# Performance work log

Hardware: AMD Instinct MI355X
Metric: run time of the kernel (lower is better)

Reference implementation:

```python
import jax, jax.numpy as jnp
import numpy as np

N_NODES = 10000
N_EDGES = 160000
BATCH = 32
IN_FEAT = 64
POLY_K = 5
OUT_FEAT = 128


def setup_inputs() -> dict:
    key = jax.random.key(0)
    k_x, k_r, k_c, k_v, k_w, k_b = jax.random.split(key, 6)
    x = jax.random.normal(k_x, (BATCH, N_NODES, IN_FEAT), dtype=jnp.float32)
    lap_rows = jax.random.randint(k_r, (N_EDGES,), 0, N_NODES, dtype=jnp.int32)
    lap_cols = jax.random.randint(k_c, (N_EDGES,), 0, N_NODES, dtype=jnp.int32)
    # small values keep the degree-5 Chebyshev recurrence numerically tame
    lap_vals = jax.random.normal(k_v, (N_EDGES,), dtype=jnp.float32) * 0.05
    weight = jax.random.normal(k_w, (IN_FEAT * POLY_K, OUT_FEAT), dtype=jnp.float32) * 0.1
    bias = jax.random.normal(k_b, (1, 1, OUT_FEAT), dtype=jnp.float32) * 0.1
    return {"x": x, "lap_rows": lap_rows, "lap_cols": lap_cols,
            "lap_vals": lap_vals, "weight": weight, "bias": bias,
            "pooling_size": 4}


def _spmm(rows, cols, vals, m):
    # sparse [N,N] @ dense [N,M] via gather + segment_sum
    return jax.ops.segment_sum(vals[:, None] * m[cols], rows, num_segments=N_NODES)


def reference(x, lap_rows, lap_cols, lap_vals, weight, bias, pooling_size):
    B, N, F = x.shape
    K = POLY_K
    Fo = weight.shape[1]
    # x0: [N, F*B]
    x0 = jnp.transpose(x, (1, 2, 0)).reshape(N, F * B)
    terms = [x0]
    if K > 1:
        x1 = _spmm(lap_rows, lap_cols, lap_vals, x0)
        terms.append(x1)
        for _ in range(2, K):
            x2 = 2.0 * _spmm(lap_rows, lap_cols, lap_vals, x1) - x0
            terms.append(x2)
            x0, x1 = x1, x2
    xk = jnp.stack(terms, axis=0)                      # [K, N, F*B]
    xk = xk.reshape(K, N, F, B)
    xk = jnp.transpose(xk, (3, 1, 2, 0))               # [B, N, F, K]
    xk = xk.reshape(B * N, F * K)
    out = (xk @ weight).reshape(B, N, Fo)              # dense projection
    out = jax.nn.relu(out + bias)                      # bias + ReLU
    if pooling_size > 1:
        out = out.reshape(B, N // pooling_size, pooling_size, Fo).max(axis=2)
    return out
```

## Files before the change

kernel.cpp:

```cpp
#include <hip/hip_runtime.h>
#include <hip/hip_bf16.h>
#include <cstddef>
#include <cstdint>

#define N_NODES 10000
#define N_EDGES 160000
#define BATCH 32
#define IN_FEAT 64
#define POLY_K 5
#define OUT_FEAT 128
#define KTOT 320
#define POOLSZ 4
#define NPOOL 2500
#define NSL 16

typedef short bf16x8 __attribute__((ext_vector_type(8)));
typedef unsigned short u16x8 __attribute__((ext_vector_type(8)));
typedef unsigned int u32x4 __attribute__((ext_vector_type(4)));
typedef float f32x4 __attribute__((ext_vector_type(4)));
typedef float f32x2 __attribute__((ext_vector_type(2)));

__device__ __forceinline__ unsigned short f2bf(float f) {
  unsigned int u = __float_as_uint(f);
  unsigned int r = u + 0x7FFFu + ((u >> 16) & 1u);
  return (unsigned short)(r >> 16);
}
__device__ __forceinline__ float bf2f(unsigned short u) {
  return __uint_as_float(((unsigned int)u) << 16);
}
__device__ __forceinline__ f32x2 unpk(unsigned int u) {
  f32x2 r;
  r[0] = __uint_as_float(u << 16);
  r[1] = __uint_as_float(u & 0xFFFF0000u);
  return r;
}


__global__ void zero_int_kernel(int* __restrict__ p, int n) {
  int i = blockIdx.x * 256 + threadIdx.x;
  if (i < n) p[i] = 0;
}

__global__ void hist_kernel(const int* __restrict__ rows, int* __restrict__ deg) {
  int e = blockIdx.x * 256 + threadIdx.x;
  if (e < N_EDGES) atomicAdd(&deg[rows[e]], 1);
}

__global__ void scan_kernel(const int* __restrict__ deg, int* __restrict__ row_start,
                            int* __restrict__ cursor) {
  __shared__ int wsum[16];
  __shared__ int carry_sm;
  int t = threadIdx.x;
  int lane = t & 63, wid = t >> 6;
  if (t == 0) { carry_sm = 0; row_start[0] = 0; }
  __syncthreads();
  for (int base = 0; base < N_NODES; base += 1024) {
    int idx = base + t;
    int v = (idx < N_NODES) ? deg[idx] : 0;
    int x = v;
    #pragma unroll
    for (int off = 1; off < 64; off <<= 1) {
      int y = __shfl_up(x, off, 64);
      if (lane >= off) x += y;
    }
    if (lane == 63) wsum[wid] = x;
    __syncthreads();
    if (wid == 0) {
      int sv = (lane < 16) ? wsum[lane] : 0;
      #pragma unroll
      for (int off = 1; off < 16; off <<= 1) {
        int y = __shfl_up(sv, off, 64);
        if (lane >= off) sv += y;
      }
      if (lane < 16) wsum[lane] = sv;
    }
    __syncthreads();
    int incl = x + (wid > 0 ? wsum[wid - 1] : 0) + carry_sm;
    if (idx < N_NODES) {
      row_start[idx + 1] = incl;
      cursor[idx] = incl - v;
    }
    __syncthreads();
    if (t == 1023) carry_sm = incl;
    __syncthreads();
  }
}

__global__ void scatter_kernel(const int* __restrict__ rows, const int* __restrict__ cols,
                               const float* __restrict__ vals, int* __restrict__ cursor,
                               int2* __restrict__ csr_pairs) {
  int e = blockIdx.x * 256 + threadIdx.x;
  if (e < N_EDGES) {
    int r = rows[e];
    int p = atomicAdd(&cursor[r], 1);
    csr_pairs[p] = make_int2(cols[e], __float_as_int(vals[e]));
  }
}


__global__ void bsort_kernel(const int* __restrict__ deg, int* __restrict__ perm) {
  int chunk = blockIdx.x * 256 + threadIdx.x;
  if (chunk >= (N_NODES + 15) / 16) return;
  int base = chunk * 16;
  int idx[16], dg[16];
  #pragma unroll
  for (int j = 0; j < 16; ++j) {
    int r = base + j;
    idx[j] = r;
    dg[j] = (r < N_NODES) ? deg[r] : 0x7fffffff;
  }
  #pragma unroll
  for (int a = 1; a < 16; ++a) {
    int dv = dg[a], iv = idx[a];
    int b = a - 1;
    while (b >= 0 && dg[b] > dv) { dg[b + 1] = dg[b]; idx[b + 1] = idx[b]; --b; }
    dg[b + 1] = dv; idx[b + 1] = iv;
  }
  #pragma unroll
  for (int j = 0; j < 16; ++j)
    if (base + j < N_NODES) perm[base + j] = idx[j];
}


__global__ void wpack_kernel(const float* __restrict__ weight, unsigned short* __restrict__ wpack) {
  int id = blockIdx.x * 256 + threadIdx.x;
  if (id >= 5120) return;
  int ft = id / 640;
  int c = (id / 64) % 10;
  int l = id % 64;
  int fo = ft * 16 + (l & 15);
  unsigned short v[8];
  #pragma unroll
  for (int j = 0; j < 8; ++j) {
    int k = c * 32 + ((l >> 4)) * 8 + j;
    int row = (k & 63) * POLY_K + (k >> 6);
    v[j] = f2bf(weight[row * OUT_FEAT + fo]);
  }
  ushort4* dst = (ushort4*)&wpack[(size_t)id * 8];
  dst[0] = make_ushort4(v[0], v[1], v[2], v[3]);
  dst[1] = make_ushort4(v[4], v[5], v[6], v[7]);
}


template <int BB>
__global__ __launch_bounds__(256) void transpose_kernel(const float* __restrict__ x,
                                                        unsigned short* __restrict__ t0, int b0) {
  constexpr int CB = 64 * BB;
  constexpr int SCOLS = CB / NSL;
  constexpr size_t SLICE_SL = (size_t)N_NODES * SCOLS;
  int n = blockIdx.x;
  int t = threadIdx.x;
  for (int i = t * 8; i < CB; i += 2048) {
    int b = i >> 6;
    int f = i & 63;
    const float* xp = &x[((size_t)(b0 + b) * N_NODES + n) * IN_FEAT + f];
    float4 v0 = *(const float4*)xp;
    float4 v1 = *(const float4*)(xp + 4);
    u16x8 o;
    o[0] = f2bf(v0.x); o[1] = f2bf(v0.y); o[2] = f2bf(v0.z); o[3] = f2bf(v0.w);
    o[4] = f2bf(v1.x); o[5] = f2bf(v1.y); o[6] = f2bf(v1.z); o[7] = f2bf(v1.w);
    int sl = i / SCOLS;
    int cw = i & (SCOLS - 1);
    *(u16x8*)&t0[(size_t)sl * SLICE_SL + (size_t)n * SCOLS + cw] = o;
  }
}


template <int BB>
__global__ __launch_bounds__(256) void spmm_kernel(const unsigned short* __restrict__ xin,
                                                   const unsigned short* __restrict__ prev,
                                                   unsigned short* __restrict__ xout,
                                                   const int* __restrict__ row_start,
                                                   const int2* __restrict__ csr_pairs,
                                                   const int* __restrict__ perm,
                                                   float alpha, int use_prev) {
  constexpr int CB = 64 * BB;
  constexpr int SCOLS = CB / NSL;
  constexpr size_t SLICE_SL = (size_t)N_NODES * SCOLS;
  constexpr int LPR = SCOLS / 8;
  constexpr int RPB = 256 / LPR;
  constexpr int RB = (N_NODES + RPB - 1) / RPB;
  constexpr int PHB = RB * 8;
  int bid = blockIdx.x;
  int phase = bid / PHB;
  int rem = bid - phase * PHB;
  int xcd = rem & 7;
  int rowblk = rem >> 3;
  int slice = phase * 8 + xcd;
  int t = threadIdx.x;
  int rl = t / LPR;
  int cl = t - rl * LPR;
  int si = rowblk * RPB + rl;
  if (si >= N_NODES) return;
  int n = perm[si];
  unsigned off = (unsigned)cl * 8u;

  const unsigned short* xs = xin  + (size_t)slice * SLICE_SL;
  const unsigned short* ps = prev + (size_t)slice * SLICE_SL;
  unsigned short*       os = xout + (size_t)slice * SLICE_SL;

  int s = row_start[n];
  int e = row_start[n + 1];
  f32x2 a0 = {0.f, 0.f}, a1 = {0.f, 0.f}, a2 = {0.f, 0.f}, a3 = {0.f, 0.f};

  int i = s;
  for (; i + 7 < e; i += 8) {
    int2 E[8];
    #pragma unroll
    for (int u = 0; u < 8; ++u) E[u] = csr_pairs[i + u];
    u32x4 d[8];
    #pragma unroll
    for (int u = 0; u < 8; ++u) d[u] = *(const u32x4*)&xs[(unsigned)E[u].x * SCOLS + off];
    #pragma unroll
    for (int u = 0; u < 8; ++u) {
      float vv = __int_as_float(E[u].y);
      f32x2 w = {vv, vv};
      a0 = __builtin_elementwise_fma(w, unpk(d[u][0]), a0);
      a1 = __builtin_elementwise_fma(w, unpk(d[u][1]), a1);
      a2 = __builtin_elementwise_fma(w, unpk(d[u][2]), a2);
      a3 = __builtin_elementwise_fma(w, unpk(d[u][3]), a3);
    }
  }
  for (; i + 3 < e; i += 4) {
    int2 E[4];
    #pragma unroll
    for (int u = 0; u < 4; ++u) E[u] = csr_pairs[i + u];
    u32x4 d[4];
    #pragma unroll
    for (int u = 0; u < 4; ++u) d[u] = *(const u32x4*)&xs[(unsigned)E[u].x * SCOLS + off];
    #pragma unroll
    for (int u = 0; u < 4; ++u) {
      float vv = __int_as_float(E[u].y);
      f32x2 w = {vv, vv};
      a0 = __builtin_elementwise_fma(w, unpk(d[u][0]), a0);
      a1 = __builtin_elementwise_fma(w, unpk(d[u][1]), a1);
      a2 = __builtin_elementwise_fma(w, unpk(d[u][2]), a2);
      a3 = __builtin_elementwise_fma(w, unpk(d[u][3]), a3);
    }
  }
  for (; i < e; ++i) {
    int2 E0 = csr_pairs[i];
    u32x4 d0 = *(const u32x4*)&xs[(unsigned)E0.x * SCOLS + off];
    float vv = __int_as_float(E0.y);
    f32x2 w0 = {vv, vv};
    a0 = __builtin_elementwise_fma(w0, unpk(d0[0]), a0);
    a1 = __builtin_elementwise_fma(w0, unpk(d0[1]), a1);
    a2 = __builtin_elementwise_fma(w0, unpk(d0[2]), a2);
    a3 = __builtin_elementwise_fma(w0, unpk(d0[3]), a3);
  }

  unsigned nelt = (unsigned)n * SCOLS + off;
  u16x8 o;
  if (use_prev) {
    u32x4 qd = *(const u32x4*)&ps[nelt];
    f32x2 q0 = unpk(qd[0]), q1 = unpk(qd[1]), q2 = unpk(qd[2]), q3 = unpk(qd[3]);
    o[0] = f2bf(alpha * a0[0] - q0[0]); o[1] = f2bf(alpha * a0[1] - q0[1]);
    o[2] = f2bf(alpha * a1[0] - q1[0]); o[3] = f2bf(alpha * a1[1] - q1[1]);
    o[4] = f2bf(alpha * a2[0] - q2[0]); o[5] = f2bf(alpha * a2[1] - q2[1]);
    o[6] = f2bf(alpha * a3[0] - q3[0]); o[7] = f2bf(alpha * a3[1] - q3[1]);
  } else {
    o[0] = f2bf(alpha * a0[0]); o[1] = f2bf(alpha * a0[1]);
    o[2] = f2bf(alpha * a1[0]); o[3] = f2bf(alpha * a1[1]);
    o[4] = f2bf(alpha * a2[0]); o[5] = f2bf(alpha * a2[1]);
    o[6] = f2bf(alpha * a3[0]); o[7] = f2bf(alpha * a3[1]);
  }
  *(u16x8*)&os[nelt] = o;
}


template <int BB>
__global__ __launch_bounds__(256, 4) void gemm_mfma_kernel(const unsigned short* __restrict__ slices,
                                                           const unsigned short* __restrict__ wpack,
                                                           const float* __restrict__ bias,
                                                           float* __restrict__ out, int b0) {
  constexpr int CB = 64 * BB;
  constexpr int SCOLS = CB / NSL;
  constexpr size_t SLICE_SL = (size_t)N_NODES * SCOLS;
  constexpr int MB = (BB >= 16) ? 16 : BB;
  constexpr int MT = MB / 4;
  constexpr int SPAN = MB * 64;
  constexpr int ROWS = 4 * MB;
  __shared__ unsigned short A[ROWS * 320];

  int g = blockIdx.x;
  int bh = blockIdx.y;
  int t = threadIdx.x;

  constexpr int CHUNKS = ROWS * 40;
  for (int idx0 = 0; idx0 < CHUNKS; idx0 += 256) {
    int idx = idx0 + t;
    int row = idx / 40;
    int cphys = idx - row * 40;
    int clog = cphys ^ (row & 7);
    int kpoly = clog >> 3;
    int fb = (clog & 7) * 8;
    int bloc = row >> 2;
    int nd = row & 3;
    int c = bh * SPAN + bloc * 64 + fb;
    int sl = c / SCOLS;
    int cw = c & (SCOLS - 1);
    const unsigned short* gsrc = &slices[((size_t)kpoly * NSL + sl) * SLICE_SL +
                                         (size_t)(g * POOLSZ + nd) * SCOLS + cw];
    unsigned short* lbase = &A[(size_t)(idx0 + (t & 192)) * 8];
    __builtin_amdgcn_global_load_lds((const __attribute__((address_space(1))) unsigned int*)gsrc,
                                     (__attribute__((address_space(3))) unsigned int*)lbase,
                                     16, 0, 0);
  }
  __syncthreads();

  int w = t >> 6;
  int l = t & 63;
  int lm = l & 15;
  int q = l >> 4;
  int swz = lm & 7;

  f32x4 acc[MT][2];
  #pragma unroll
  for (int mt = 0; mt < MT; ++mt)
    #pragma unroll
    for (int fj = 0; fj < 2; ++fj) {
      acc[mt][fj][0] = 0.f; acc[mt][fj][1] = 0.f;
      acc[mt][fj][2] = 0.f; acc[mt][fj][3] = 0.f;
    }

  #pragma unroll
  for (int c = 0; c < 10; ++c) {
    bf16x8 bfrag[2];
    #pragma unroll
    for (int fj = 0; fj < 2; ++fj) {
      int fi = w * 2 + fj;
      bfrag[fj] = *(const bf16x8*)&wpack[(size_t)(((fi * 10) + c) * 64 + l) * 8];
    }
    #pragma unroll
    for (int mt = 0; mt < MT; ++mt) {
      bf16x8 afrag = *(const bf16x8*)&A[(mt * 16 + lm) * 320 + (((c * 4 + q) ^ swz) << 3)];
      acc[mt][0] = __builtin_amdgcn_mfma_f32_16x16x32_bf16(afrag, bfrag[0], acc[mt][0], 0, 0, 0);
      acc[mt][1] = __builtin_amdgcn_mfma_f32_16x16x32_bf16(afrag, bfrag[1], acc[mt][1], 0, 0, 0);
    }
  }

  #pragma unroll
  for (int fj = 0; fj < 2; ++fj) {
    int fo = (w * 2 + fj) * 16 + lm;
    float bv = bias[fo];
    #pragma unroll
    for (int mt = 0; mt < MT; ++mt) {
      float mx = fmaxf(fmaxf(acc[mt][fj][0], acc[mt][fj][1]),
                       fmaxf(acc[mt][fj][2], acc[mt][fj][3]));
      float val = fmaxf(mx + bv, 0.f);
      int b = b0 + bh * MB + mt * 4 + q;
      out[((size_t)b * NPOOL + g) * OUT_FEAT + fo] = val;
    }
  }
}


template <int BB>
static void run_pipeline(const float* x, const float* bias,
                         const int* row_start, const int2* csr_pairs, const int* perm,
                         const unsigned short* wpack,
                         unsigned short* slices, float* out, hipStream_t stream) {
  constexpr int CB = 64 * BB;
  constexpr size_t TERM = (size_t)N_NODES * CB;
  constexpr int LPR = (CB / NSL) / 8;
  constexpr int RPB = 256 / LPR;
  constexpr int NBLK = ((N_NODES + RPB - 1) / RPB) * NSL;
  constexpr int MB = (BB >= 16) ? 16 : BB;
  for (int b0 = 0; b0 < BATCH; b0 += BB) {
    transpose_kernel<BB><<<N_NODES, 256, 0, stream>>>(x, slices, b0);
    for (int k = 1; k < POLY_K; ++k) {
      const unsigned short* xin  = slices + (size_t)(k - 1) * TERM;
      const unsigned short* prev = (k >= 2) ? slices + (size_t)(k - 2) * TERM : slices;
      unsigned short* xout = slices + (size_t)k * TERM;
      float alpha = (k == 1) ? 1.0f : 2.0f;
      spmm_kernel<BB><<<NBLK, 256, 0, stream>>>(xin, prev, xout, row_start,
                                                csr_pairs, perm, alpha,
                                                (k >= 2) ? 1 : 0);
    }
    gemm_mfma_kernel<BB><<<dim3(NPOOL, BB / MB), 256, 0, stream>>>(slices, wpack, bias, out, b0);
  }
}

static size_t needed_bytes(int BB) {
  return 1522176u + (size_t)6400000 * BB;
}

extern "C" void kernel_launch(void* const* d_in, const int* in_sizes, int n_in,
                              void* d_out, int out_size, void* d_ws, size_t ws_size,
                              hipStream_t stream) {
  const float* x        = (const float*)d_in[0];
  const int*   lap_rows = (const int*)d_in[1];
  const int*   lap_cols = (const int*)d_in[2];
  const float* lap_vals = (const float*)d_in[3];
  const float* weight   = (const float*)d_in[4];
  const float* bias     = (const float*)d_in[5];
  float* out = (float*)d_out;

  int* deg       = (int*)d_ws;
  int* cursor    = deg + 10016;
  int* row_start = cursor + 10016;
  int* perm      = row_start + 10016;
  int2* csr_pairs = (int2*)(perm + 10016);
  unsigned short* wpack = (unsigned short*)(csr_pairs + N_EDGES);
  unsigned short* slices = wpack + 40960;

  int BB = 0;
  if      (ws_size >= needed_bytes(32)) BB = 32;
  else if (ws_size >= needed_bytes(16)) BB = 16;
  else if (ws_size >= needed_bytes(8))  BB = 8;
  else if (ws_size >= needed_bytes(4))  BB = 4;
  if (BB == 0) return;

  zero_int_kernel<<<(N_NODES + 255) / 256, 256, 0, stream>>>(deg, N_NODES);
  hist_kernel<<<(N_EDGES + 255) / 256, 256, 0, stream>>>(lap_rows, deg);
  scan_kernel<<<1, 1024, 0, stream>>>(deg, row_start, cursor);
  scatter_kernel<<<(N_EDGES + 255) / 256, 256, 0, stream>>>(lap_rows, lap_cols, lap_vals,
                                                            cursor, csr_pairs);
  bsort_kernel<<<3, 256, 0, stream>>>(deg, perm);
  wpack_kernel<<<20, 256, 0, stream>>>(weight, wpack);

  switch (BB) {
    case 32: run_pipeline<32>(x, bias, row_start, csr_pairs, perm, wpack, slices, out, stream); break;
    case 16: run_pipeline<16>(x, bias, row_start, csr_pairs, perm, wpack, slices, out, stream); break;
    case 8:  run_pipeline<8>(x, bias, row_start, csr_pairs, perm, wpack, slices, out, stream); break;
    case 4:  run_pipeline<4>(x, bias, row_start, csr_pairs, perm, wpack, slices, out, stream); break;
  }
}
```

Before: 424.5 us.

## Split GEMM LDS staging into two phases and batch nodes per transpose block

The GEMM kernel's shared-memory A tile is reorganised into per-polynomial-term planes, each 64 columns wide. When MB is 16, the first two terms are staged and synced, and their MFMAs run while the remaining terms are still loading, so part of the global-to-LDS latency overlaps with compute. Weight fragments for the first chunks are also prefetched. Separately, the transpose kernel now handles 8 nodes per block with a fixed thread-to-(batch, node, feature) mapping, which cuts the block count and gives each thread more work. The extra phase and barrier add complexity, and the untested non-16 path also had to be rewritten to the new layout.

```diff
diff --git a/kernel.cpp b/kernel.cpp
--- a/kernel.cpp
+++ b/kernel.cpp
@@ -148,20 +148,26 @@
   constexpr int CB = 64 * BB;
   constexpr int SCOLS = CB / NSL;
   constexpr size_t SLICE_SL = (size_t)N_NODES * SCOLS;
-  int n = blockIdx.x;
+  constexpr int NN = 8;
+  int n0 = blockIdx.x * NN;
   int t = threadIdx.x;
-  for (int i = t * 8; i < CB; i += 2048) {
-    int b = i >> 6;
-    int f = i & 63;
-    const float* xp = &x[((size_t)(b0 + b) * N_NODES + n) * IN_FEAT + f];
+  int bsub = t >> 6;
+  int n = (t >> 3) & 7;
+  int f8 = t & 7;
+  int node = n0 + n;
+  #pragma unroll
+  for (int bi = 0; bi < BB / 4; ++bi) {
+    int b = bi * 4 + bsub;
+    const float* xp = &x[((size_t)(b0 + b) * N_NODES + node) * IN_FEAT + f8 * 8];
     float4 v0 = *(const float4*)xp;
     float4 v1 = *(const float4*)(xp + 4);
     u16x8 o;
     o[0] = f2bf(v0.x); o[1] = f2bf(v0.y); o[2] = f2bf(v0.z); o[3] = f2bf(v0.w);
     o[4] = f2bf(v1.x); o[5] = f2bf(v1.y); o[6] = f2bf(v1.z); o[7] = f2bf(v1.w);
+    int i = b * 64 + f8 * 8;
     int sl = i / SCOLS;
-    int cw = i & (SCOLS - 1);
-    *(u16x8*)&t0[(size_t)sl * SLICE_SL + (size_t)n * SCOLS + cw] = o;
+    int cw = i - sl * SCOLS;
+    *(u16x8*)&t0[(size_t)sl * SLICE_SL + (size_t)node * SCOLS + cw] = o;
   }
 }
 
@@ -280,20 +286,21 @@
   constexpr int MT = MB / 4;
   constexpr int SPAN = MB * 64;
   constexpr int ROWS = 4 * MB;
-  __shared__ unsigned short A[ROWS * 320];
+  constexpr int CHUNKS = ROWS * 40;
+  __shared__ unsigned short A[POLY_K * ROWS * 64];
 
   int g = blockIdx.x;
   int bh = blockIdx.y;
   int t = threadIdx.x;
 
-  constexpr int CHUNKS = ROWS * 40;
-  for (int idx0 = 0; idx0 < CHUNKS; idx0 += 256) {
+  auto stage = [&](int idx0) {
     int idx = idx0 + t;
-    int row = idx / 40;
-    int cphys = idx - row * 40;
-    int clog = cphys ^ (row & 7);
-    int kpoly = clog >> 3;
-    int fb = (clog & 7) * 8;
+    int kpoly = idx / (ROWS * 8);
+    int rem = idx - kpoly * (ROWS * 8);
+    int row = rem >> 3;
+    int cphys = idx & 7;
+    int clog3 = cphys ^ (row & 7);
+    int fb = clog3 * 8;
     int bloc = row >> 2;
     int nd = row & 3;
     int c = bh * SPAN + bloc * 64 + fb;
@@ -305,8 +312,7 @@
     __builtin_amdgcn_global_load_lds((const __attribute__((address_space(1))) unsigned int*)gsrc,
                                      (__attribute__((address_space(3))) unsigned int*)lbase,
                                      16, 0, 0);
-  }
-  __syncthreads();
+  };
 
   int w = t >> 6;
   int l = t & 63;
@@ -323,19 +329,58 @@
       acc[mt][fj][2] = 0.f; acc[mt][fj][3] = 0.f;
     }
 
-  #pragma unroll
-  for (int c = 0; c < 10; ++c) {
-    bf16x8 bfrag[2];
-    #pragma unroll
-    for (int fj = 0; fj < 2; ++fj) {
-      int fi = w * 2 + fj;
-      bfrag[fj] = *(const bf16x8*)&wpack[(size_t)(((fi * 10) + c) * 64 + l) * 8];
-    }
-    #pragma unroll
-    for (int mt = 0; mt < MT; ++mt) {
-      bf16x8 afrag = *(const bf16x8*)&A[(mt * 16 + lm) * 320 + (((c * 4 + q) ^ swz) << 3)];
-      acc[mt][0] = __builtin_amdgcn_mfma_f32_16x16x32_bf16(afrag, bfrag[0], acc[mt][0], 0, 0, 0);
-      acc[mt][1] = __builtin_amdgcn_mfma_f32_16x16x32_bf16(afrag, bfrag[1], acc[mt][1], 0, 0, 0);
+  if constexpr (MB == 16) {
+    constexpr int PH1 = 2 * ROWS * 8;
+    for (int idx0 = 0; idx0 < PH1; idx0 += 256) stage(idx0);
+    bf16x8 bpre[4][2];
+    #pragma unroll
+    for (int c = 0; c < 4; ++c)
+      #pragma unroll
+      for (int fj = 0; fj < 2; ++fj)
+        bpre[c][fj] = *(const bf16x8*)&wpack[(size_t)((((w * 2 + fj) * 10) + c) * 64 + l) * 8];
+    __syncthreads();
+    for (int idx0 = PH1; idx0 < CHUNKS; idx0 += 256) stage(idx0);
+    #pragma unroll
+    for (int c = 0; c < 4; ++c) {
+      #pragma unroll
+      for (int mt = 0; mt < MT; ++mt) {
+        bf16x8 afrag = *(const bf16x8*)
+            &A[((c >> 1) * ROWS + mt * 16 + lm) * 64 + ((((c & 1) * 4 + q) ^ swz) << 3)];
+        acc[mt][0] = __builtin_amdgcn_mfma_f32_16x16x32_bf16(afrag, bpre[c][0], acc[mt][0], 0, 0, 0);
+        acc[mt][1] = __builtin_amdgcn_mfma_f32_16x16x32_bf16(afrag, bpre[c][1], acc[mt][1], 0, 0, 0);
+      }
+    }
+    __syncthreads();
+    #pragma unroll
+    for (int c = 4; c < 10; ++c) {
+      bf16x8 bfrag[2];
+      #pragma unroll
+      for (int fj = 0; fj < 2; ++fj)
+        bfrag[fj] = *(const bf16x8*)&wpack[(size_t)((((w * 2 + fj) * 10) + c) * 64 + l) * 8];
+      #pragma unroll
+      for (int mt = 0; mt < MT; ++mt) {
+        bf16x8 afrag = *(const bf16x8*)
+            &A[((c >> 1) * ROWS + mt * 16 + lm) * 64 + ((((c & 1) * 4 + q) ^ swz) << 3)];
+        acc[mt][0] = __builtin_amdgcn_mfma_f32_16x16x32_bf16(afrag, bfrag[0], acc[mt][0], 0, 0, 0);
+        acc[mt][1] = __builtin_amdgcn_mfma_f32_16x16x32_bf16(afrag, bfrag[1], acc[mt][1], 0, 0, 0);
+      }
+    }
+  } else {
+    for (int idx0 = 0; idx0 < CHUNKS; idx0 += 256) stage(idx0);
+    __syncthreads();
+    #pragma unroll
+    for (int c = 0; c < 10; ++c) {
+      bf16x8 bfrag[2];
+      #pragma unroll
+      for (int fj = 0; fj < 2; ++fj)
+        bfrag[fj] = *(const bf16x8*)&wpack[(size_t)((((w * 2 + fj) * 10) + c) * 64 + l) * 8];
+      #pragma unroll
+      for (int mt = 0; mt < MT; ++mt) {
+        bf16x8 afrag = *(const bf16x8*)
+            &A[((c >> 1) * ROWS + mt * 16 + lm) * 64 + ((((c & 1) * 4 + q) ^ swz) << 3)];
+        acc[mt][0] = __builtin_amdgcn_mfma_f32_16x16x32_bf16(afrag, bfrag[0], acc[mt][0], 0, 0, 0);
+        acc[mt][1] = __builtin_amdgcn_mfma_f32_16x16x32_bf16(afrag, bfrag[1], acc[mt][1], 0, 0, 0);
+      }
     }
   }
 
@@ -367,7 +412,7 @@
   constexpr int NBLK = ((N_NODES + RPB - 1) / RPB) * NSL;
   constexpr int MB = (BB >= 16) ? 16 : BB;
   for (int b0 = 0; b0 < BATCH; b0 += BB) {
-    transpose_kernel<BB><<<N_NODES, 256, 0, stream>>>(x, slices, b0);
+    transpose_kernel<BB><<<N_NODES / 8, 256, 0, stream>>>(x, slices, b0);
     for (int k = 1; k < POLY_K; ++k) {
       const unsigned short* xin  = slices + (size_t)(k - 1) * TERM;
       const unsigned short* prev = (k >= 2) ? slices + (size_t)(k - 2) * TERM : slices;
```

Measured after the change: 417.1 us, median of 2. No clear change (-1.7%).
